# Optimization experiments

Hardware: AMD Instinct MI355X
Metric: run time of the kernel (lower is better)

## Reference

```python
import jax, jax.numpy as jnp
import numpy as np

N_NODES = 50000
N_EDGES = 800000
FEAT = 128
HID = 128
N_GRAPHS = 512
N_CLASSES = 10
N_BLOCKS = 3
N_INNER = 2
BN_EPS = 1e-5


def setup_inputs() -> dict:
    key = jax.random.key(0)
    ks = jax.random.split(key, 16)
    return {
        "x": jax.random.normal(ks[0], (N_NODES, FEAT), dtype=jnp.float32),
        "edge_attr": jax.random.uniform(ks[1], (N_EDGES,), dtype=jnp.float32),
        "conv_w": jax.random.normal(ks[2], (N_BLOCKS, N_INNER, HID, HID), dtype=jnp.float32) * 0.05,
        "conv_b": jax.random.normal(ks[3], (N_BLOCKS, N_INNER, HID), dtype=jnp.float32) * 0.05,
        "jk_w": jax.random.normal(ks[4], (N_BLOCKS, N_INNER * HID, HID), dtype=jnp.float32) * 0.05,
        "jk_b": jax.random.normal(ks[5], (N_BLOCKS, HID), dtype=jnp.float32) * 0.05,
        "bn_gamma": jnp.ones((N_BLOCKS * HID,), dtype=jnp.float32),
        "bn_beta": jnp.zeros((N_BLOCKS * HID,), dtype=jnp.float32),
        "bn_mean": jnp.zeros((N_BLOCKS * HID,), dtype=jnp.float32),
        "bn_var": jnp.ones((N_BLOCKS * HID,), dtype=jnp.float32),
        "lin1_w": jax.random.normal(ks[6], (N_BLOCKS * HID, HID), dtype=jnp.float32) * 0.05,
        "lin1_b": jnp.zeros((HID,), dtype=jnp.float32),
        "lin2_w": jax.random.normal(ks[7], (HID, N_CLASSES), dtype=jnp.float32) * 0.05,
        "lin2_b": jnp.zeros((N_CLASSES,), dtype=jnp.float32),
        "edge_index": jax.random.randint(ks[8], (2, N_EDGES), 0, N_NODES, dtype=jnp.int32),
        "batch": jnp.sort(jax.random.randint(ks[9], (N_NODES,), 0, N_GRAPHS, dtype=jnp.int32)),
    }


def _gcn_conv(x, w, b, src, dst, ew):
    """GCNConv with edge weights and self-loops: D^-1/2 (A+I) D^-1/2 X W + b."""
    n = x.shape[0]
    xw = x @ w  # [N, H]
    deg = jax.ops.segment_sum(ew, dst, num_segments=n) + 1.0  # self-loop weight 1
    dinv = jax.lax.rsqrt(deg)  # [N]
    norm = dinv[src] * ew * dinv[dst]  # [E]
    agg = jax.ops.segment_sum(xw[src] * norm[:, None], dst, num_segments=n)
    agg = agg + xw * (dinv * dinv)[:, None]  # self-loop term
    return agg + b


def reference(x, edge_attr, conv_w, conv_b, jk_w, jk_b, bn_gamma, bn_beta,
              bn_mean, bn_var, lin1_w, lin1_b, lin2_w, lin2_b,
              edge_index, batch):
    src, dst = edge_index[0], edge_index[1]
    h = x
    pooled = []
    for l in range(N_BLOCKS):
        xs = []
        for k in range(N_INNER):
            h = jax.nn.relu(_gcn_conv(h, conv_w[l, k], conv_b[l, k], src, dst, edge_attr))
            xs.append(h)
        # JumpingKnowledge 'cat' + Linear + ReLU
        h = jax.nn.relu(jnp.concatenate(xs, axis=-1) @ jk_w[l] + jk_b[l])
        # global add pool per graph
        pooled.append(jax.ops.segment_sum(h, batch, num_segments=N_GRAPHS))
    z = jnp.concatenate(pooled, axis=1)  # [B, 3*HID]
    # BatchNorm1d (eval mode)
    z = (z - bn_mean) * jax.lax.rsqrt(bn_var + BN_EPS) * bn_gamma + bn_beta
    z = jax.nn.relu(z @ lin1_w + lin1_b)
    z = z @ lin2_w + lin2_b
    return jax.nn.softmax(z, axis=-1)
```

## Files before the change

kernel.cpp:

```cpp
#include <hip/hip_runtime.h>

static constexpr int NN = 50000;
static constexpr int NE = 800000;
static constexpr int NG = 512;

typedef unsigned int uint;
typedef unsigned short ushort;
typedef unsigned long long u64;
typedef __attribute__((ext_vector_type(8))) short short8;
typedef __attribute__((ext_vector_type(4))) float f32x4;

__device__ inline uint bfbits(float f) {
    uint u = __float_as_uint(f);
    return (u + 0x7fffu + ((u >> 16) & 1u)) >> 16;
}
__device__ inline float bflo(uint g) { return __uint_as_float(g << 16); }
__device__ inline float bfhi(uint g) { return __uint_as_float(g & 0xffff0000u); }
__device__ inline float bf2f(ushort s) { return __uint_as_float(((uint)s) << 16); }

__global__ void hist_kernel(const int* __restrict__ dst, const float* __restrict__ ew,
                            u64* __restrict__ pk, int nE)
{
    int i = blockIdx.x * blockDim.x + threadIdx.x;
    if (i < nE) {
        int d = dst[i];
        u64 v = (1ULL << 40) + (u64)(ew[i] * 16777216.0f + 0.5f);
        atomicAdd(&pk[d], v);
    }
}

__global__ __launch_bounds__(256) void scan_bsum_kernel(const u64* __restrict__ pk,
                                                        int* __restrict__ bsum,
                                                        float* __restrict__ dinv, int n)
{
    __shared__ int wred[4];
    int i = blockIdx.x * 256 + threadIdx.x;
    int v = 0;
    if (i < n) {
        u64 p = pk[i];
        v = (int)(p >> 40);
        float deg = (float)(p & 0xFFFFFFFFFFULL) * (1.0f / 16777216.0f) + 1.0f;
        dinv[i] = rsqrtf(deg);
    }
    int s = v;
    #pragma unroll
    for (int o = 32; o > 0; o >>= 1) s += __shfl_down(s, o, 64);
    int wid = threadIdx.x >> 6;
    if ((threadIdx.x & 63) == 0) wred[wid] = s;
    __syncthreads();
    if (threadIdx.x == 0)
        bsum[blockIdx.x] = wred[0] + wred[1] + wred[2] + wred[3];
}

__global__ __launch_bounds__(256) void scan_boff_kernel(const int* __restrict__ bsum,
                                                        int* __restrict__ boff, int nbs)
{
    __shared__ int sh[256];
    int tid = threadIdx.x;
    int v = (tid < nbs) ? bsum[tid] : 0;
    sh[tid] = v;
    __syncthreads();
    #pragma unroll
    for (int o = 1; o < 256; o <<= 1) {
        int t = (tid >= o) ? sh[tid - o] : 0;
        __syncthreads();
        sh[tid] += t;
        __syncthreads();
    }
    if (tid < nbs) boff[tid] = sh[tid] - v;
    if (tid == 255) boff[nbs] = sh[255];
}

__global__ __launch_bounds__(256) void scan_final_kernel(const u64* __restrict__ pk,
                                                         const int* __restrict__ boff,
                                                         int* __restrict__ rowptr,
                                                         int n, int nbs)
{
    __shared__ int sh[256];
    int tid = threadIdx.x;
    int i = blockIdx.x * 256 + tid;
    int v = (i < n) ? (int)(pk[i] >> 40) : 0;
    sh[tid] = v;
    __syncthreads();
    #pragma unroll
    for (int o = 1; o < 256; o <<= 1) {
        int t = (tid >= o) ? sh[tid - o] : 0;
        __syncthreads();
        sh[tid] += t;
        __syncthreads();
    }
    if (i < n) rowptr[i] = boff[blockIdx.x] + sh[tid] - v;
    if (blockIdx.x == 0 && tid == 0) rowptr[n] = boff[nbs];
}

__global__ void fill_kernel(const int* __restrict__ src, const int* __restrict__ dst,
                            const float* __restrict__ ew, const float* __restrict__ dinv,
                            const int* __restrict__ rowptr, int* __restrict__ cursor,
                            uint2* __restrict__ ecv, int nE)
{
    int i = blockIdx.x * blockDim.x + threadIdx.x;
    if (i < nE) {
        int s = src[i], d = dst[i];
        int pos = rowptr[d] + atomicAdd(&cursor[d], 1);
        uint2 cv;
        cv.x = (uint)s;
        cv.y = __float_as_uint(ew[i] * dinv[s]);
        ecv[pos] = cv;
    }
}

__global__ void cvtx_kernel(const float* __restrict__ x, ushort* __restrict__ xb, int n)
{
    int i = (blockIdx.x * blockDim.x + threadIdx.x) * 4;
    if (i < n) {
        float4 v = *(const float4*)&x[i];
        uint2 p;
        p.x = bfbits(v.x) | (bfbits(v.y) << 16);
        p.y = bfbits(v.z) | (bfbits(v.w) << 16);
        *(uint2*)&xb[i] = p;
    }
}

__global__ void wfrag_kernel(const float* __restrict__ src, ushort* __restrict__ dst,
                             int K, int wstride_src, int wstride_dst)
{
    int wid = blockIdx.y;
    const float* s = src + (size_t)wid * wstride_src;
    ushort* d = dst + (size_t)wid * wstride_dst;
    int i = blockIdx.x * 256 + threadIdx.x;
    int e = i & 7;
    int lane = (i >> 3) & 63;
    int rest = i >> 9;
    int nt = K >> 5;
    int t = rest % nt;
    int j = rest / nt;
    int k = t * 32 + (lane >> 4) * 8 + e;
    int col = j * 16 + (lane & 15);
    d[i] = (ushort)bfbits(s[(size_t)k * 128 + col]);
}

template<bool RELU, bool BIAS>
__global__ __launch_bounds__(256) void gemm_mfma_kernel(
    const ushort* __restrict__ Ab, int K, int lda,
    const ushort* __restrict__ Wb, const float* __restrict__ bias,
    ushort* __restrict__ outb, int nrows)
{
    const int wid  = threadIdx.x >> 6;
    const int lane = threadIdx.x & 63;
    const int row0 = blockIdx.x * 64 + wid * 16;
    const int c    = lane & 15;
    const int kg   = lane >> 4;
    int arow = row0 + c;
    if (arow >= nrows) arow = nrows - 1;
    const ushort* Aptr = Ab + (size_t)arow * lda + kg * 8;
    const int nt = K >> 5;

    f32x4 acc[8];
    #pragma unroll
    for (int j = 0; j < 8; ++j) acc[j] = (f32x4)0.f;

    for (int t = 0; t < nt; ++t) {
        short8 a = *(const short8*)(Aptr + t * 32);
        const ushort* Wp = Wb + ((size_t)t * 64 + lane) * 8;
        #pragma unroll
        for (int j = 0; j < 8; ++j) {
            short8 b = *(const short8*)(Wp + (size_t)j * nt * 512);
            acc[j] = __builtin_amdgcn_mfma_f32_16x16x32_bf16(a, b, acc[j], 0, 0, 0);
        }
    }
    #pragma unroll
    for (int r = 0; r < 4; ++r) {
        int orow = row0 + kg * 4 + r;
        if (orow >= nrows) continue;
        #pragma unroll
        for (int j = 0; j < 8; ++j) {
            float v = acc[j][r];
            int col = j * 16 + c;
            if (BIAS) v += bias[col];
            if (RELU) v = fmaxf(v, 0.f);
            outb[(size_t)orow * 128 + col] = (ushort)bfbits(v);
        }
    }
}

__global__ __launch_bounds__(256) void agg_kernel(
    const uint* __restrict__ xwb, const int* __restrict__ rowptr,
    const uint2* __restrict__ ecv,
    const float* __restrict__ dinv, const float* __restrict__ bias,
    uint* __restrict__ outu, int ldo, int coff, int n)
{
    int node = (int)((blockIdx.x * (size_t)blockDim.x + threadIdx.x) >> 6);
    int lane = threadIdx.x & 63;
    if (node >= n) return;
    float d = dinv[node];
    uint  g = xwb[(size_t)node * 64 + lane];
    float bx = 0.f, by = 0.f;
    int e0 = rowptr[node], e1 = rowptr[node + 1];
    int e = e0;
    for (; e + 8 <= e1; e += 8) {
        uint2 cv[8];
        #pragma unroll
        for (int q = 0; q < 8; ++q) cv[q] = ecv[e + q];
        uint gq[8];
        #pragma unroll
        for (int q = 0; q < 8; ++q) gq[q] = xwb[(size_t)cv[q].x * 64 + lane];
        #pragma unroll
        for (int q = 0; q < 8; ++q) {
            float v = __uint_as_float(cv[q].y);
            bx = fmaf(v, bflo(gq[q]), bx);
            by = fmaf(v, bfhi(gq[q]), by);
        }
    }
    for (; e + 4 <= e1; e += 4) {
        uint2 cv[4];
        #pragma unroll
        for (int q = 0; q < 4; ++q) cv[q] = ecv[e + q];
        uint gq[4];
        #pragma unroll
        for (int q = 0; q < 4; ++q) gq[q] = xwb[(size_t)cv[q].x * 64 + lane];
        #pragma unroll
        for (int q = 0; q < 4; ++q) {
            float v = __uint_as_float(cv[q].y);
            bx = fmaf(v, bflo(gq[q]), bx);
            by = fmaf(v, bfhi(gq[q]), by);
        }
    }
    for (; e < e1; ++e) {
        uint2 cv = ecv[e];
        uint gg = xwb[(size_t)cv.x * 64 + lane];
        float v = __uint_as_float(cv.y);
        bx = fmaf(v, bflo(gg), bx);
        by = fmaf(v, bfhi(gg), by);
    }
    float sw = d * d;
    float ax = fmaf(d, bx, bflo(g) * sw);
    float ay = fmaf(d, by, bfhi(g) * sw);
    float2 b = *(const float2*)&bias[lane * 2];
    ax = fmaxf(ax + b.x, 0.f);
    ay = fmaxf(ay + b.y, 0.f);
    outu[(size_t)node * ldo + coff + lane] = bfbits(ax) | (bfbits(ay) << 16);
}

static constexpr int NPP = 32;
__global__ __launch_bounds__(128) void pool_kernel(
    const ushort* __restrict__ h, const int* __restrict__ batch,
    float* __restrict__ z, int zoff, int n)
{
    int f  = threadIdx.x;
    int n0 = blockIdx.x * NPP;
    if (n0 >= n) return;
    int nend = n0 + NPP; if (nend > n) nend = n;
    int cur = batch[n0];
    float acc = 0.f;
    for (int node = n0; node < nend; ++node) {
        int b = batch[node];
        if (b != cur) {
            atomicAdd(&z[(size_t)cur * 384 + zoff + f], acc);
            acc = 0.f; cur = b;
        }
        acc += bf2f(h[(size_t)node * 128 + f]);
    }
    atomicAdd(&z[(size_t)cur * 384 + zoff + f], acc);
}

__global__ __launch_bounds__(128) void head_kernel(
    const float* __restrict__ z,
    const float* __restrict__ g,  const float* __restrict__ be,
    const float* __restrict__ mu, const float* __restrict__ var,
    const float* __restrict__ w1, const float* __restrict__ b1,
    const float* __restrict__ w2, const float* __restrict__ b2,
    float* __restrict__ out)
{
    int gi = blockIdx.x;
    int t  = threadIdx.x;
    __shared__ float zs[384];
    __shared__ float h1[128];
    __shared__ float lg[10];
    for (int i = t; i < 384; i += 128) {
        float v = z[(size_t)gi * 384 + i];
        v = (v - mu[i]) * rsqrtf(var[i] + 1e-5f) * g[i] + be[i];
        zs[i] = v;
    }
    __syncthreads();
    float acc = b1[t];
    for (int k = 0; k < 384; ++k) acc = fmaf(zs[k], w1[(size_t)k * 128 + t], acc);
    h1[t] = fmaxf(acc, 0.f);
    __syncthreads();
    if (t < 10) {
        float a2 = b2[t];
        for (int k = 0; k < 128; ++k) a2 = fmaf(h1[k], w2[(size_t)k * 10 + t], a2);
        lg[t] = a2;
    }
    __syncthreads();
    if (t == 0) {
        float m = lg[0];
        for (int i = 1; i < 10; ++i) m = fmaxf(m, lg[i]);
        float e[10], s = 0.f;
        for (int i = 0; i < 10; ++i) { e[i] = expf(lg[i] - m); s += e[i]; }
        float inv = 1.f / s;
        for (int i = 0; i < 10; ++i) out[(size_t)gi * 10 + i] = e[i] * inv;
    }
}

extern "C" void kernel_launch(void* const* d_in, const int* in_sizes, int n_in,
                              void* d_out, int out_size, void* d_ws, size_t ws_size,
                              hipStream_t stream)
{
    const float* x      = (const float*)d_in[0];
    const float* ea     = (const float*)d_in[1];
    const float* conv_w = (const float*)d_in[2];
    const float* conv_b = (const float*)d_in[3];
    const float* jk_w   = (const float*)d_in[4];
    const float* jk_b   = (const float*)d_in[5];
    const float* bn_g   = (const float*)d_in[6];
    const float* bn_b   = (const float*)d_in[7];
    const float* bn_m   = (const float*)d_in[8];
    const float* bn_v   = (const float*)d_in[9];
    const float* w1     = (const float*)d_in[10];
    const float* b1     = (const float*)d_in[11];
    const float* w2     = (const float*)d_in[12];
    const float* b2     = (const float*)d_in[13];
    const int*   eidx   = (const int*)d_in[14];
    const int*   batch  = (const int*)d_in[15];
    const int* srcv = eidx;
    const int* dstv = eidx + NE;
    float* out = (float*)d_out;

    char* ws = (char*)d_ws;
    size_t off = 0;
    auto alloc = [&](size_t b) { size_t o = off; off += (b + 511) & ~(size_t)511; return o; };
    u64*   pk     = (u64*)  (ws + alloc((size_t)NN * 8));
    int*   cursor = (int*)  (ws + alloc((size_t)NN * 4));
    float* z      = (float*)(ws + alloc((size_t)NG * 384 * 4));
    size_t zero_bytes = off;
    float* dinv   = (float*)(ws + alloc((size_t)NN * 4));
    int*   rowptr = (int*)  (ws + alloc((size_t)(NN + 1) * 4));
    uint2* ecv    = (uint2*)(ws + alloc((size_t)NE * 8));
    ushort* xb    = (ushort*)(ws + alloc((size_t)NN * 128 * 2));
    ushort* wbc   = (ushort*)(ws + alloc((size_t)6 * 128 * 128 * 2));
    ushort* wbj   = (ushort*)(ws + alloc((size_t)3 * 256 * 128 * 2));
    uint*  xwb    = (uint*) (ws + alloc((size_t)NN * 64 * 4));
    uint*  xsb    = (uint*) (ws + alloc((size_t)NN * 128 * 4));
    ushort* houtb = (ushort*)(ws + alloc((size_t)NN * 128 * 2));
    int*   bsum   = (int*)  (ws + alloc((size_t)256 * 4));
    int*   boff   = (int*)  (ws + alloc((size_t)257 * 4));
    (void)ws_size; (void)in_sizes; (void)n_in; (void)out_size;

    hipMemsetAsync(d_ws, 0, zero_bytes, stream);

    const int EB  = (NE + 255) / 256;
    const int NB  = (NN + 255) / 256;
    hist_kernel<<<EB, 256, 0, stream>>>(dstv, ea, pk, NE);
    scan_bsum_kernel<<<NB, 256, 0, stream>>>(pk, bsum, dinv, NN);
    scan_boff_kernel<<<1, 256, 0, stream>>>(bsum, boff, NB);
    scan_final_kernel<<<NB, 256, 0, stream>>>(pk, boff, rowptr, NN, NB);
    fill_kernel<<<EB, 256, 0, stream>>>(srcv, dstv, ea, dinv, rowptr, cursor,
                                        ecv, NE);
    cvtx_kernel<<<(NN * 32 + 255) / 256, 256, 0, stream>>>(x, xb, NN * 128);
    wfrag_kernel<<<dim3(64, 6),  256, 0, stream>>>(conv_w, wbc, 128, 128 * 128, 128 * 128);
    wfrag_kernel<<<dim3(128, 3), 256, 0, stream>>>(jk_w,   wbj, 256, 256 * 128, 256 * 128);

    const int GB = (NN + 63) / 64;
    const int AB = (NN * 64 + 255) / 256;
    const int PB = (NN + NPP - 1) / NPP;

    const ushort* hin = xb;
    int lda = 128;
    for (int l = 0; l < 3; ++l) {
        for (int k = 0; k < 2; ++k) {
            gemm_mfma_kernel<false, false><<<GB, 256, 0, stream>>>(
                hin, 128, lda, wbc + (size_t)(l * 2 + k) * 128 * 128, nullptr,
                (ushort*)xwb, NN);
            agg_kernel<<<AB, 256, 0, stream>>>(
                xwb, rowptr, ecv, dinv, conv_b + (size_t)(l * 2 + k) * 128,
                xsb, 128, k * 64, NN);
            hin = (const ushort*)xsb;
            lda = 256;
        }
        gemm_mfma_kernel<true, true><<<GB, 256, 0, stream>>>(
            (const ushort*)xsb, 256, 256, wbj + (size_t)l * 256 * 128,
            jk_b + (size_t)l * 128, houtb, NN);
        pool_kernel<<<PB, 128, 0, stream>>>(houtb, batch, z, l * 128, NN);
        hin = houtb;
        lda = 128;
    }
    head_kernel<<<NG, 128, 0, stream>>>(z, bn_g, bn_b, bn_m, bn_v,
                                        w1, b1, w2, b2, out);
}
```

Before: 618.6 us.

## Pack CSR edges into 32-bit records and reuse histogram atomic ranks

Each CSR edge record shrinks from 8 bytes (int src plus float weight) to 4 bytes: a 16-bit source index and an fp16 normalised weight. This halves edge-stream traffic in the six aggregation passes. The fill kernel also drops its second atomic pass, reading each edge's slot from the return value of the histogram atomic instead. The 16-bit source field truncates node ids above 65535, which is wrong for 50000 nodes (ids up to 49999 fit, so it holds here), and the fp16 weights lose precision.

```diff
diff --git a/kernel.cpp b/kernel.cpp
--- a/kernel.cpp
+++ b/kernel.cpp
@@ -1,4 +1,5 @@
 #include <hip/hip_runtime.h>
+#include <hip/hip_fp16.h>
 
 static constexpr int NN = 50000;
 static constexpr int NE = 800000;
@@ -19,13 +20,14 @@
 __device__ inline float bf2f(ushort s) { return __uint_as_float(((uint)s) << 16); }
 
 __global__ void hist_kernel(const int* __restrict__ dst, const float* __restrict__ ew,
-                            u64* __restrict__ pk, int nE)
+                            u64* __restrict__ pk, ushort* __restrict__ rankb, int nE)
 {
     int i = blockIdx.x * blockDim.x + threadIdx.x;
     if (i < nE) {
         int d = dst[i];
         u64 v = (1ULL << 40) + (u64)(ew[i] * 16777216.0f + 0.5f);
-        atomicAdd(&pk[d], v);
+        u64 old = atomicAdd(&pk[d], v);
+        rankb[i] = (ushort)(old >> 40);
     }
 }
 
@@ -95,17 +97,16 @@
 
 __global__ void fill_kernel(const int* __restrict__ src, const int* __restrict__ dst,
                             const float* __restrict__ ew, const float* __restrict__ dinv,
-                            const int* __restrict__ rowptr, int* __restrict__ cursor,
-                            uint2* __restrict__ ecv, int nE)
+                            const int* __restrict__ rowptr,
+                            const ushort* __restrict__ rankb,
+                            uint* __restrict__ ecv, int nE)
 {
     int i = blockIdx.x * blockDim.x + threadIdx.x;
     if (i < nE) {
         int s = src[i], d = dst[i];
-        int pos = rowptr[d] + atomicAdd(&cursor[d], 1);
-        uint2 cv;
-        cv.x = (uint)s;
-        cv.y = __float_as_uint(ew[i] * dinv[s]);
-        ecv[pos] = cv;
+        int pos = rowptr[d] + (int)rankb[i];
+        float v = ew[i] * dinv[s];
+        ecv[pos] = (uint)s | ((uint)__half_as_ushort(__float2half_rn(v)) << 16);
     }
 }
 
@@ -185,7 +186,7 @@
 
 __global__ __launch_bounds__(256) void agg_kernel(
     const uint* __restrict__ xwb, const int* __restrict__ rowptr,
-    const uint2* __restrict__ ecv,
+    const uint* __restrict__ ecv,
     const float* __restrict__ dinv, const float* __restrict__ bias,
     uint* __restrict__ outu, int ldo, int coff, int n)
 {
@@ -198,37 +199,39 @@
     int e0 = rowptr[node], e1 = rowptr[node + 1];
     int e = e0;
     for (; e + 8 <= e1; e += 8) {
-        uint2 cv[8];
-        #pragma unroll
-        for (int q = 0; q < 8; ++q) cv[q] = ecv[e + q];
+        uint rec[8];
+        #pragma unroll
+        for (int q = 0; q < 8; ++q) rec[q] = ecv[e + q];
         uint gq[8];
         #pragma unroll
-        for (int q = 0; q < 8; ++q) gq[q] = xwb[(size_t)cv[q].x * 64 + lane];
+        for (int q = 0; q < 8; ++q)
+            gq[q] = xwb[(size_t)(rec[q] & 0xffffu) * 64 + lane];
         #pragma unroll
         for (int q = 0; q < 8; ++q) {
-            float v = __uint_as_float(cv[q].y);
+            float v = __half2float(__ushort_as_half((ushort)(rec[q] >> 16)));
             bx = fmaf(v, bflo(gq[q]), bx);
             by = fmaf(v, bfhi(gq[q]), by);
         }
     }
     for (; e + 4 <= e1; e += 4) {
-        uint2 cv[4];
-        #pragma unroll
-        for (int q = 0; q < 4; ++q) cv[q] = ecv[e + q];
+        uint rec[4];
+        #pragma unroll
+        for (int q = 0; q < 4; ++q) rec[q] = ecv[e + q];
         uint gq[4];
         #pragma unroll
-        for (int q = 0; q < 4; ++q) gq[q] = xwb[(size_t)cv[q].x * 64 + lane];
+        for (int q = 0; q < 4; ++q)
+            gq[q] = xwb[(size_t)(rec[q] & 0xffffu) * 64 + lane];
         #pragma unroll
         for (int q = 0; q < 4; ++q) {
-            float v = __uint_as_float(cv[q].y);
+            float v = __half2float(__ushort_as_half((ushort)(rec[q] >> 16)));
             bx = fmaf(v, bflo(gq[q]), bx);
             by = fmaf(v, bfhi(gq[q]), by);
         }
     }
     for (; e < e1; ++e) {
-        uint2 cv = ecv[e];
-        uint gg = xwb[(size_t)cv.x * 64 + lane];
-        float v = __uint_as_float(cv.y);
+        uint rec = ecv[e];
+        uint gg = xwb[(size_t)(rec & 0xffffu) * 64 + lane];
+        float v = __half2float(__ushort_as_half((ushort)(rec >> 16)));
         bx = fmaf(v, bflo(gg), bx);
         by = fmaf(v, bfhi(gg), by);
     }
@@ -330,12 +333,12 @@
     size_t off = 0;
     auto alloc = [&](size_t b) { size_t o = off; off += (b + 511) & ~(size_t)511; return o; };
     u64*   pk     = (u64*)  (ws + alloc((size_t)NN * 8));
-    int*   cursor = (int*)  (ws + alloc((size_t)NN * 4));
     float* z      = (float*)(ws + alloc((size_t)NG * 384 * 4));
     size_t zero_bytes = off;
     float* dinv   = (float*)(ws + alloc((size_t)NN * 4));
     int*   rowptr = (int*)  (ws + alloc((size_t)(NN + 1) * 4));
-    uint2* ecv    = (uint2*)(ws + alloc((size_t)NE * 8));
+    ushort* rankb = (ushort*)(ws + alloc((size_t)NE * 2));
+    uint*  ecv    = (uint*) (ws + alloc((size_t)NE * 4));
     ushort* xb    = (ushort*)(ws + alloc((size_t)NN * 128 * 2));
     ushort* wbc   = (ushort*)(ws + alloc((size_t)6 * 128 * 128 * 2));
     ushort* wbj   = (ushort*)(ws + alloc((size_t)3 * 256 * 128 * 2));
@@ -350,11 +353,11 @@
 
     const int EB  = (NE + 255) / 256;
     const int NB  = (NN + 255) / 256;
-    hist_kernel<<<EB, 256, 0, stream>>>(dstv, ea, pk, NE);
+    hist_kernel<<<EB, 256, 0, stream>>>(dstv, ea, pk, rankb, NE);
     scan_bsum_kernel<<<NB, 256, 0, stream>>>(pk, bsum, dinv, NN);
     scan_boff_kernel<<<1, 256, 0, stream>>>(bsum, boff, NB);
     scan_final_kernel<<<NB, 256, 0, stream>>>(pk, boff, rowptr, NN, NB);
-    fill_kernel<<<EB, 256, 0, stream>>>(srcv, dstv, ea, dinv, rowptr, cursor,
+    fill_kernel<<<EB, 256, 0, stream>>>(srcv, dstv, ea, dinv, rowptr, rankb,
                                         ecv, NE);
     cvtx_kernel<<<(NN * 32 + 255) / 256, 256, 0, stream>>>(x, xb, NN * 128);
     wfrag_kernel<<<dim3(64, 6),  256, 0, stream>>>(conv_w, wbc, 128, 128 * 128, 128 * 128);
```

New measurement: 588.6 us. -4.9%, faster.
